# Performance work log

Hardware: AMD Instinct MI355X
Metric: run time of the kernel (lower is better)

Reference implementation:

```python
import jax, jax.numpy as jnp
import numpy as np

B, S, D, H = 32, 1024, 256, 256


def setup_inputs() -> dict:
    key = jax.random.key(0)
    ks = jax.random.split(key, 7)
    s_in = 1.0 / np.sqrt(D)
    s_h = 1.0 / np.sqrt(H)
    x = jax.random.normal(ks[0], (B, S, D), dtype=jnp.float32)
    # gate order: i, f, g, o stacked along last dim -> 4H
    W_fwd = jax.random.uniform(ks[1], (D, 4 * H), dtype=jnp.float32, minval=-s_in, maxval=s_in)
    U_fwd = jax.random.uniform(ks[2], (H, 4 * H), dtype=jnp.float32, minval=-s_h, maxval=s_h)
    b_fwd = jax.random.uniform(ks[3], (4 * H,), dtype=jnp.float32, minval=-s_in, maxval=s_in)
    W_rev = jax.random.uniform(ks[4], (D, 4 * H), dtype=jnp.float32, minval=-s_in, maxval=s_in)
    U_rev = jax.random.uniform(ks[5], (H, 4 * H), dtype=jnp.float32, minval=-s_h, maxval=s_h)
    b_rev = jax.random.uniform(ks[6], (4 * H,), dtype=jnp.float32, minval=-s_in, maxval=s_in)
    return {"x": x, "W_fwd": W_fwd, "U_fwd": U_fwd, "b_fwd": b_fwd,
            "W_rev": W_rev, "U_rev": U_rev, "b_rev": b_rev}


def _lstm_scan(x, W, U, b):
    # x: [B, S, D] -> outputs h over time: [B, S, H]
    hdim = U.shape[0]
    # precompute input projection for all steps: [S, B, 4H]
    xW = jnp.einsum('bsd,dg->sbg', x, W) + b

    def step(carry, xw_t):
        h, c = carry
        gates = xw_t + h @ U  # [B, 4H]
        i_t = jax.nn.sigmoid(gates[:, 0 * hdim:1 * hdim])
        f_t = jax.nn.sigmoid(gates[:, 1 * hdim:2 * hdim])
        g_t = jnp.tanh(gates[:, 2 * hdim:3 * hdim])
        o_t = jax.nn.sigmoid(gates[:, 3 * hdim:4 * hdim])
        c_t = f_t * c + i_t * g_t
        h_t = o_t * jnp.tanh(c_t)
        return (h_t, c_t), h_t

    bsz = x.shape[0]
    h0 = jnp.zeros((bsz, hdim), dtype=x.dtype)
    c0 = jnp.zeros((bsz, hdim), dtype=x.dtype)
    _, hs = jax.lax.scan(step, (h0, c0), xW)
    return jnp.transpose(hs, (1, 0, 2))  # [B, S, H]


def reference(x, W_fwd, U_fwd, b_fwd, W_rev, U_rev, b_rev):
    out_f = _lstm_scan(x, W_fwd, U_fwd, b_fwd)
    out_r = _lstm_scan(x[:, ::-1, :], W_rev, U_rev, b_rev)[:, ::-1, :]
    return jnp.concatenate([out_f, out_r], axis=2)  # [B, S, 2H]
```

## Files before the change

kernel.cpp:

```cpp
#include <hip/hip_runtime.h>
#include <hip/hip_bf16.h>

typedef _Float16 f16;
typedef _Float16 half8 __attribute__((ext_vector_type(8)));
typedef float f32x4 __attribute__((ext_vector_type(4)));
typedef int i32x4 __attribute__((ext_vector_type(4)));


__global__ void prep_uq_kernel(const float* __restrict__ Uf, const float* __restrict__ Ur,
                               unsigned int* __restrict__ UQm, float* __restrict__ Uscale)
{
    int idx = blockIdx.x * 256 + threadIdx.x;
    if (idx >= 2048) return;
    int dir = idx >> 10, c = idx & 1023;
    const float* U = dir ? Ur : Uf;
    float m = 0.f;
    for (int k = 0; k < 256; ++k) m = fmaxf(m, fabsf(U[k * 1024 + c]));
    float sinv = (m > 0.f) ? 127.f / m : 0.f;
    int tile = c >> 4, colr = c & 15;
    uint4* UQm4 = (uint4*)UQm;
    for (int ks = 0; ks < 4; ++ks) {
        #pragma unroll
        for (int kg = 0; kg < 4; ++kg) {
            unsigned int w[4];
            #pragma unroll
            for (int d = 0; d < 4; ++d) {
                unsigned int wd = 0;
                #pragma unroll
                for (int e = 0; e < 4; ++e) {
                    int k = ks * 64 + kg * 16 + d * 4 + e;
                    int q = __float2int_rn(U[k * 1024 + c] * sinv);
                    wd |= ((unsigned int)(q & 0xff)) << (8 * e);
                }
                w[d] = wd;
            }
            UQm4[((size_t)((dir * 64 + tile) * 4 + ks)) * 64 + kg * 16 + colr] =
                make_uint4(w[0], w[1], w[2], w[3]);
        }
    }
    Uscale[idx] = m / (127.f * 127.f);
}

__global__ __launch_bounds__(256) void proj_gemm_kernel(
    const float* __restrict__ x, const float* __restrict__ Wf, const float* __restrict__ Wr,
    const float* __restrict__ bfw, const float* __restrict__ brw, f16* __restrict__ G)
{
    const int nt = blockIdx.x;
    const int mt = blockIdx.y;
    const int m0 = mt * 128, n0 = nt * 128;
    const int dir = n0 >> 10, nin0 = n0 & 1023;
    const float* W   = dir ? Wr : Wf;
    const float* bia = dir ? brw : bfw;
    __shared__ f16 Asm[128][40];
    __shared__ f16 Bsm[128][40];
    const int t = threadIdx.x;
    const int lane = t & 63, wave = t >> 6;
    const int wr = wave >> 1, wc = wave & 1;
    f32x4 acc[4][4] = {};
    for (int k0 = 0; k0 < 256; k0 += 32) {
        #pragma unroll
        for (int e = 0; e < 16; ++e) {
            int idx = e * 256 + t;
            int r = idx >> 5, kk = idx & 31;
            Asm[r][kk] = (f16)x[(size_t)(m0 + r) * 256 + (k0 + kk)];
        }
        #pragma unroll
        for (int e = 0; e < 16; ++e) {
            int idx = e * 256 + t;
            int col = idx & 127, kr = idx >> 7;
            Bsm[col][kr] = (f16)W[(size_t)(k0 + kr) * 1024 + (nin0 + col)];
        }
        __syncthreads();
        const int l15 = lane & 15, kb = (lane >> 4) * 8;
        half8 af[4], bfr[4];
        #pragma unroll
        for (int fr = 0; fr < 4; ++fr) af[fr]  = *(const half8*)&Asm[wr * 64 + fr * 16 + l15][kb];
        #pragma unroll
        for (int fc = 0; fc < 4; ++fc) bfr[fc] = *(const half8*)&Bsm[wc * 64 + fc * 16 + l15][kb];
        #pragma unroll
        for (int fr = 0; fr < 4; ++fr)
            #pragma unroll
            for (int fc = 0; fc < 4; ++fc)
                acc[fr][fc] = __builtin_amdgcn_mfma_f32_16x16x32_f16(af[fr], bfr[fc], acc[fr][fc], 0, 0, 0);
        __syncthreads();
    }
    const int row4 = (lane >> 4) * 4, c15 = lane & 15;
    #pragma unroll
    for (int fr = 0; fr < 4; ++fr)
        #pragma unroll
        for (int fc = 0; fc < 4; ++fc) {
            int rbase = m0 + wr * 64 + fr * 16 + row4;
            int cidx  = n0 + wc * 64 + fc * 16 + c15;
            float bv = bia[cidx & 1023];
            #pragma unroll
            for (int i = 0; i < 4; ++i)
                G[(size_t)(rbase + i) * 2048 + cidx] = (f16)(acc[fr][fc][i] + bv);
        }
}

template<int PAT>
__device__ __forceinline__ float qb(float v) {
    return __int_as_float(__builtin_amdgcn_mov_dpp(__float_as_int(v), PAT, 0xF, 0xF, true));
}

#define LGKM_BARRIER() do { \
    asm volatile("s_waitcnt lgkmcnt(0)\n\ts_barrier" ::: "memory"); \
    __builtin_amdgcn_sched_barrier(0); \
} while (0)

__global__
__attribute__((amdgpu_flat_work_group_size(1024, 1024)))
__attribute__((amdgpu_waves_per_eu(4, 4)))
void scan_kernel(
    const f16* __restrict__ G, const unsigned int* __restrict__ UQm,
    const float* __restrict__ Uscale, float* __restrict__ out)
{
    const int wg = blockIdx.x;
    const int dir = wg >> 5, b = wg & 31;
    const int tid = threadIdx.x;
    const int wave = tid >> 6, lane = tid & 63;
    const int colq = lane >> 2, gate = lane & 3;
    const int mycol = wave * 16 + colq;

    __shared__ __align__(16) unsigned int hq[128];

    if (tid < 64) hq[tid] = 0u;

    const i32x4* UQm4 = (const i32x4*)UQm;
    i32x4 uf0[4], uf1[4], uf2[4], uf3[4];
    #pragma unroll
    for (int ks = 0; ks < 4; ++ks) {
        uf0[ks] = UQm4[((size_t)((dir * 64 + ( 0 + wave)) * 4 + ks)) * 64 + lane];
        uf1[ks] = UQm4[((size_t)((dir * 64 + (16 + wave)) * 4 + ks)) * 64 + lane];
        uf2[ks] = UQm4[((size_t)((dir * 64 + (32 + wave)) * 4 + ks)) * 64 + lane];
        uf3[ks] = UQm4[((size_t)((dir * 64 + (48 + wave)) * 4 + ks)) * 64 + lane];
    }

    const float uscl = Uscale[dir * 1024 + gate * 256 + mycol];

    const f16* Gl = G + (size_t)b * 1024 * 2048 + dir * 1024 + gate * 256 + mycol;
    float* outp = out + (size_t)b * 1024 * 512 + dir * 256 + mycol;

    const int s0 = dir ? 1023 : 0;
    float xw = (float)Gl[(size_t)s0 * 2048];
    float c_state = 0.f;
    __syncthreads();

    const char* hqb = (const char*)hq;
    signed char* hqw = (signed char*)hq;
    const int arow = (lane >> 4) << 4;
    const int baddr = lane & ~3;
    int p = 0;

    for (int t = 0; t < 1024; ++t) {
        const int s  = dir ? (1023 - t) : t;
        const int tn = (t < 1023) ? (t + 1) : t;
        const int sn = dir ? (1023 - tn) : tn;
        f16 xn = Gl[(size_t)sn * 2048];

        i32x4 acc0 = {0,0,0,0}, acc1 = {0,0,0,0}, acc2 = {0,0,0,0}, acc3 = {0,0,0,0};
        #pragma unroll
        for (int ks = 0; ks < 4; ++ks) {
            i32x4 a = *(const i32x4*)(hqb + p * 256 + ks * 64 + arow);
            acc0 = __builtin_amdgcn_mfma_i32_16x16x64_i8(a, uf0[ks], acc0, 0, 0, 0);
            acc1 = __builtin_amdgcn_mfma_i32_16x16x64_i8(a, uf1[ks], acc1, 0, 0, 0);
            acc2 = __builtin_amdgcn_mfma_i32_16x16x64_i8(a, uf2[ks], acc2, 0, 0, 0);
            acc3 = __builtin_amdgcn_mfma_i32_16x16x64_i8(a, uf3[ks], acc3, 0, 0, 0);
        }

        int r0 = __builtin_amdgcn_ds_bpermute(baddr, acc0[0]);
        int r1 = __builtin_amdgcn_ds_bpermute(baddr, acc1[0]);
        int r2 = __builtin_amdgcn_ds_bpermute(baddr, acc2[0]);
        int r3 = __builtin_amdgcn_ds_bpermute(baddr, acc3[0]);
        int iv01 = (gate & 1) ? r1 : r0;
        int iv23 = (gate & 1) ? r3 : r2;
        int iv   = (gate & 2) ? iv23 : iv01;

        float pre = (float)iv * uscl + xw;
        float a2 = (gate == 2) ? (pre + pre) : -pre;
        float E  = __expf(a2);
        float r  = __fdividef(1.f, E + 1.f);
        float v  = (gate == 2) ? (1.f - 2.f * r) : r;
        float b0 = qb<0x00>(v), b1 = qb<0x55>(v), b2 = qb<0xAA>(v), b3 = qb<0xFF>(v);
        c_state = b1 * c_state + b0 * b2;
        float e2 = __expf(c_state + c_state);
        float th = 1.f - __fdividef(2.f, e2 + 1.f);
        float h  = b3 * th;

        if (gate == 0) outp[(size_t)s * 512] = h;
        if (gate == 1) hqw[(p ^ 1) * 256 + mycol] = (signed char)__float2int_rn(h * 127.f);

        LGKM_BARRIER();
        p ^= 1;
        xw = (float)xn;
    }
}

extern "C" void kernel_launch(void* const* d_in, const int* in_sizes, int n_in,
                              void* d_out, int out_size, void* d_ws, size_t ws_size,
                              hipStream_t stream) {
    const float* x  = (const float*)d_in[0];
    const float* Wf = (const float*)d_in[1];
    const float* Uf = (const float*)d_in[2];
    const float* bf = (const float*)d_in[3];
    const float* Wr = (const float*)d_in[4];
    const float* Ur = (const float*)d_in[5];
    const float* br = (const float*)d_in[6];
    float* out = (float*)d_out;

    char* ws = (char*)d_ws;
    unsigned int* UQm = (unsigned int*)ws;
    float* Uscale     = (float*)(ws + (size_t)512 * 1024);
    f16* G            = (f16*)(ws + (size_t)1024 * 1024);

    prep_uq_kernel<<<8, 256, 0, stream>>>(Uf, Ur, UQm, Uscale);
    dim3 gg(16, 256);
    proj_gemm_kernel<<<gg, 256, 0, stream>>>(x, Wf, Wr, bf, br, G);
    scan_kernel<<<64, 1024, 0, stream>>>(G, UQm, Uscale, out);
}
```

Baseline: 1.021 ms.

## Split recurrent matvec between MFMA waves and sdot4 VALU waves

Waves 0-11 keep computing their hidden columns with int8 MFMA. Waves 12-15 now compute their 64 hidden columns per gate with packed int8 dot4 instructions on the VALU, using a separate per-column weight layout that the prep kernel now writes. The aim is to take load off the shared matrix unit on each step of the serial scan by moving part of the work to the vector ALUs. In exchange, the VALU waves carry a longer dependent dot chain and read the full h vector from LDS every step, which may make them the slowest path before the barrier.

New measurement: 1.255 ms. 22.9% more time.

```diff
diff --git a/kernel.cpp b/kernel.cpp
--- a/kernel.cpp
+++ b/kernel.cpp
@@ -8,7 +8,8 @@
 
 
 __global__ void prep_uq_kernel(const float* __restrict__ Uf, const float* __restrict__ Ur,
-                               unsigned int* __restrict__ UQm, float* __restrict__ Uscale)
+                               unsigned int* __restrict__ UQm, unsigned int* __restrict__ UQd,
+                               float* __restrict__ Uscale)
 {
     int idx = blockIdx.x * 256 + threadIdx.x;
     if (idx >= 2048) return;
@@ -36,6 +37,19 @@
             }
             UQm4[((size_t)((dir * 64 + tile) * 4 + ks)) * 64 + kg * 16 + colr] =
                 make_uint4(w[0], w[1], w[2], w[3]);
+        }
+    }
+    int g = c >> 8, hc = c & 255;
+    if (hc >= 192) {
+        int cc = g * 64 + (hc - 192);
+        for (int kk = 0; kk < 64; ++kk) {
+            unsigned int wd = 0;
+            #pragma unroll
+            for (int e = 0; e < 4; ++e) {
+                int q = __float2int_rn(U[(kk * 4 + e) * 1024 + c] * sinv);
+                wd |= ((unsigned int)(q & 0xff)) << (8 * e);
+            }
+            UQd[((size_t)(dir * 256 + cc)) * 64 + kk] = wd;
         }
     }
     Uscale[idx] = m / (127.f * 127.f);
@@ -98,6 +112,18 @@
         }
 }
 
+__device__ __forceinline__ int dot4i8(unsigned int a, unsigned int b, int c) {
+#if __has_builtin(__builtin_amdgcn_sdot4)
+    return __builtin_amdgcn_sdot4(a, b, c, false);
+#else
+    c += (int)(signed char)(a)       * (int)(signed char)(b);
+    c += (int)(signed char)(a >> 8)  * (int)(signed char)(b >> 8);
+    c += (int)(signed char)(a >> 16) * (int)(signed char)(b >> 16);
+    c += (int)(signed char)(a >> 24) * (int)(signed char)(b >> 24);
+    return c;
+#endif
+}
+
 template<int PAT>
 __device__ __forceinline__ float qb(float v) {
     return __int_as_float(__builtin_amdgcn_mov_dpp(__float_as_int(v), PAT, 0xF, 0xF, true));
@@ -113,34 +139,41 @@
 __attribute__((amdgpu_waves_per_eu(4, 4)))
 void scan_kernel(
     const f16* __restrict__ G, const unsigned int* __restrict__ UQm,
-    const float* __restrict__ Uscale, float* __restrict__ out)
+    const unsigned int* __restrict__ UQd, const float* __restrict__ Uscale,
+    float* __restrict__ out)
 {
     const int wg = blockIdx.x;
     const int dir = wg >> 5, b = wg & 31;
     const int tid = threadIdx.x;
     const int wave = tid >> 6, lane = tid & 63;
+    const bool mw = (wave < 12);
     const int colq = lane >> 2, gate = lane & 3;
-    const int mycol = wave * 16 + colq;
+    const int hc = mw ? (wave * 16 + colq) : (192 + (wave - 12) * 16 + colq);
 
     __shared__ __align__(16) unsigned int hq[128];
-
     if (tid < 64) hq[tid] = 0u;
 
-    const i32x4* UQm4 = (const i32x4*)UQm;
-    i32x4 uf0[4], uf1[4], uf2[4], uf3[4];
-    #pragma unroll
-    for (int ks = 0; ks < 4; ++ks) {
-        uf0[ks] = UQm4[((size_t)((dir * 64 + ( 0 + wave)) * 4 + ks)) * 64 + lane];
-        uf1[ks] = UQm4[((size_t)((dir * 64 + (16 + wave)) * 4 + ks)) * 64 + lane];
-        uf2[ks] = UQm4[((size_t)((dir * 64 + (32 + wave)) * 4 + ks)) * 64 + lane];
-        uf3[ks] = UQm4[((size_t)((dir * 64 + (48 + wave)) * 4 + ks)) * 64 + lane];
-    }
-
-    const float uscl = Uscale[dir * 1024 + gate * 256 + mycol];
-
-    const f16* Gl = G + (size_t)b * 1024 * 2048 + dir * 1024 + gate * 256 + mycol;
-    float* outp = out + (size_t)b * 1024 * 512 + dir * 256 + mycol;
-
+    i32x4 ub[16];
+    if (mw) {
+        const i32x4* UQm4 = (const i32x4*)UQm;
+        #pragma unroll
+        for (int g = 0; g < 4; ++g)
+            #pragma unroll
+            for (int ks = 0; ks < 4; ++ks)
+                ub[g * 4 + ks] =
+                    UQm4[((size_t)((dir * 64 + g * 16 + wave) * 4 + ks)) * 64 + lane];
+    } else {
+        const int cc = gate * 64 + (wave - 12) * 16 + colq;
+        const i32x4* up = (const i32x4*)(UQd + ((size_t)(dir * 256 + cc)) * 64);
+        #pragma unroll
+        for (int kkk = 0; kkk < 16; ++kkk)
+            ub[kkk] = up[kkk];
+    }
+
+    const float uscl = Uscale[dir * 1024 + gate * 256 + hc];
+
+    const f16* Gl = G + (size_t)b * 1024 * 2048 + dir * 1024 + gate * 256 + hc;
+    float* outp = out + (size_t)b * 1024 * 512 + dir * 256 + hc;
     const int s0 = dir ? 1023 : 0;
     float xw = (float)Gl[(size_t)s0 * 2048];
     float c_state = 0.f;
@@ -158,25 +191,57 @@
         const int sn = dir ? (1023 - tn) : tn;
         f16 xn = Gl[(size_t)sn * 2048];
 
-        i32x4 acc0 = {0,0,0,0}, acc1 = {0,0,0,0}, acc2 = {0,0,0,0}, acc3 = {0,0,0,0};
-        #pragma unroll
-        for (int ks = 0; ks < 4; ++ks) {
-            i32x4 a = *(const i32x4*)(hqb + p * 256 + ks * 64 + arow);
-            acc0 = __builtin_amdgcn_mfma_i32_16x16x64_i8(a, uf0[ks], acc0, 0, 0, 0);
-            acc1 = __builtin_amdgcn_mfma_i32_16x16x64_i8(a, uf1[ks], acc1, 0, 0, 0);
-            acc2 = __builtin_amdgcn_mfma_i32_16x16x64_i8(a, uf2[ks], acc2, 0, 0, 0);
-            acc3 = __builtin_amdgcn_mfma_i32_16x16x64_i8(a, uf3[ks], acc3, 0, 0, 0);
-        }
-
-        int r0 = __builtin_amdgcn_ds_bpermute(baddr, acc0[0]);
-        int r1 = __builtin_amdgcn_ds_bpermute(baddr, acc1[0]);
-        int r2 = __builtin_amdgcn_ds_bpermute(baddr, acc2[0]);
-        int r3 = __builtin_amdgcn_ds_bpermute(baddr, acc3[0]);
-        int iv01 = (gate & 1) ? r1 : r0;
-        int iv23 = (gate & 1) ? r3 : r2;
-        int iv   = (gate & 2) ? iv23 : iv01;
-
-        float pre = (float)iv * uscl + xw;
+        float pre;
+        if (mw) {
+            i32x4 acc0 = {0,0,0,0}, acc1 = {0,0,0,0}, acc2 = {0,0,0,0}, acc3 = {0,0,0,0};
+            #pragma unroll
+            for (int ks = 0; ks < 4; ++ks) {
+                i32x4 a = *(const i32x4*)(hqb + p * 256 + ks * 64 + arow);
+                acc0 = __builtin_amdgcn_mfma_i32_16x16x64_i8(a, ub[ 0 + ks], acc0, 0, 0, 0);
+                acc1 = __builtin_amdgcn_mfma_i32_16x16x64_i8(a, ub[ 4 + ks], acc1, 0, 0, 0);
+                acc2 = __builtin_amdgcn_mfma_i32_16x16x64_i8(a, ub[ 8 + ks], acc2, 0, 0, 0);
+                acc3 = __builtin_amdgcn_mfma_i32_16x16x64_i8(a, ub[12 + ks], acc3, 0, 0, 0);
+            }
+            int r0 = __builtin_amdgcn_ds_bpermute(baddr, acc0[0]);
+            int r1 = __builtin_amdgcn_ds_bpermute(baddr, acc1[0]);
+            int r2 = __builtin_amdgcn_ds_bpermute(baddr, acc2[0]);
+            int r3 = __builtin_amdgcn_ds_bpermute(baddr, acc3[0]);
+            int iv01 = (gate & 1) ? r1 : r0;
+            int iv23 = (gate & 1) ? r3 : r2;
+            int iv   = (gate & 2) ? iv23 : iv01;
+            pre = (float)iv * uscl + xw;
+        } else {
+            const uint4* hp4 = (const uint4*)(hqb + p * 256);
+            int i0 = 0, i1 = 0, i2 = 0, i3 = 0;
+            #pragma unroll
+            for (int ch = 0; ch < 4; ++ch) {
+                uint4 ha = hp4[ch * 4 + 0];
+                uint4 hb = hp4[ch * 4 + 1];
+                uint4 hcv = hp4[ch * 4 + 2];
+                uint4 hd = hp4[ch * 4 + 3];
+                const i32x4 u0 = ub[ch * 4 + 0], u1 = ub[ch * 4 + 1];
+                const i32x4 u2 = ub[ch * 4 + 2], u3 = ub[ch * 4 + 3];
+                i0 = dot4i8((unsigned)u0[0], ha.x, i0);
+                i1 = dot4i8((unsigned)u0[1], ha.y, i1);
+                i2 = dot4i8((unsigned)u0[2], ha.z, i2);
+                i3 = dot4i8((unsigned)u0[3], ha.w, i3);
+                i0 = dot4i8((unsigned)u1[0], hb.x, i0);
+                i1 = dot4i8((unsigned)u1[1], hb.y, i1);
+                i2 = dot4i8((unsigned)u1[2], hb.z, i2);
+                i3 = dot4i8((unsigned)u1[3], hb.w, i3);
+                i0 = dot4i8((unsigned)u2[0], hcv.x, i0);
+                i1 = dot4i8((unsigned)u2[1], hcv.y, i1);
+                i2 = dot4i8((unsigned)u2[2], hcv.z, i2);
+                i3 = dot4i8((unsigned)u2[3], hcv.w, i3);
+                i0 = dot4i8((unsigned)u3[0], hd.x, i0);
+                i1 = dot4i8((unsigned)u3[1], hd.y, i1);
+                i2 = dot4i8((unsigned)u3[2], hd.z, i2);
+                i3 = dot4i8((unsigned)u3[3], hd.w, i3);
+                __builtin_amdgcn_sched_barrier(0);
+            }
+            pre = (float)((i0 + i1) + (i2 + i3)) * uscl + xw;
+        }
+
         float a2 = (gate == 2) ? (pre + pre) : -pre;
         float E  = __expf(a2);
         float r  = __fdividef(1.f, E + 1.f);
@@ -188,7 +253,7 @@
         float h  = b3 * th;
 
         if (gate == 0) outp[(size_t)s * 512] = h;
-        if (gate == 1) hqw[(p ^ 1) * 256 + mycol] = (signed char)__float2int_rn(h * 127.f);
+        if (gate == 1) hqw[(p ^ 1) * 256 + hc] = (signed char)__float2int_rn(h * 127.f);
 
         LGKM_BARRIER();
         p ^= 1;
@@ -210,11 +275,12 @@
 
     char* ws = (char*)d_ws;
     unsigned int* UQm = (unsigned int*)ws;
-    float* Uscale     = (float*)(ws + (size_t)512 * 1024);
+    unsigned int* UQd = (unsigned int*)(ws + (size_t)512 * 1024);
+    float* Uscale     = (float*)(ws + (size_t)768 * 1024);
     f16* G            = (f16*)(ws + (size_t)1024 * 1024);
 
-    prep_uq_kernel<<<8, 256, 0, stream>>>(Uf, Ur, UQm, Uscale);
+    prep_uq_kernel<<<8, 256, 0, stream>>>(Uf, Ur, UQm, UQd, Uscale);
     dim3 gg(16, 256);
     proj_gemm_kernel<<<gg, 256, 0, stream>>>(x, Wf, Wr, bf, br, G);
-    scan_kernel<<<64, 1024, 0, stream>>>(G, UQm, Uscale, out);
-}
+    scan_kernel<<<64, 1024, 0, stream>>>(G, UQm, UQd, Uscale, out);
+}
```
